# Performance work log

Measured on AMD Instinct MI355X. Metric: run time of the kernel, lower is better.

The kernel has to match this reference:

```python
import jax, jax.numpy as jnp
import numpy as np

EMBED_DIM = 384
HEADS = 6
HEAD_DIM = EMBED_DIM // HEADS
WINDOW = 64


def setup_inputs() -> dict:
    key = jax.random.key(0)
    ks = jax.random.split(key, 5)
    B, T = 128, 256
    s_attn = 1.0 / np.sqrt(EMBED_DIM)
    x = jax.random.normal(ks[0], (B, T, EMBED_DIM), dtype=jnp.float32)
    W_attn = jax.random.normal(ks[1], (EMBED_DIM, 3 * EMBED_DIM), dtype=jnp.float32) * s_attn
    b_attn = jax.random.normal(ks[2], (3 * EMBED_DIM,), dtype=jnp.float32) * 0.02
    W_proj = jax.random.normal(ks[3], (EMBED_DIM, EMBED_DIM), dtype=jnp.float32) * s_attn
    b_proj = jax.random.normal(ks[4], (EMBED_DIM,), dtype=jnp.float32) * 0.02
    return {"x": x, "W_attn": W_attn, "b_attn": b_attn, "W_proj": W_proj, "b_proj": b_proj}


def reference(x, W_attn, b_attn, W_proj, b_proj):
    B, T, C = x.shape
    qkv = x @ W_attn + b_attn  # [B,T,3C]
    q, k, v = jnp.split(qkv, 3, axis=-1)
    # [B, H, T, hd]
    q = q.reshape(B, T, HEADS, HEAD_DIM).transpose(0, 2, 1, 3)
    k = k.reshape(B, T, HEADS, HEAD_DIM).transpose(0, 2, 1, 3)
    v = v.reshape(B, T, HEADS, HEAD_DIM).transpose(0, 2, 1, 3)
    scale = 1.0 / np.sqrt(HEAD_DIM).astype(np.float32)
    att = jnp.einsum('bhqd,bhkd->bhqk', q, k) * scale
    i = jnp.arange(T)
    causal = i[:, None] >= i[None, :]
    local = jnp.abs(i[:, None] - i[None, :]) <= WINDOW
    mask = (causal & local)[None, None, :, :]
    att = jnp.where(mask, att, -jnp.inf)
    att = jax.nn.softmax(att, axis=-1)
    y = jnp.einsum('bhqk,bhkd->bhqd', att, v)
    y = y.transpose(0, 2, 1, 3).reshape(B, T, C)
    return y @ W_proj + b_proj
```

## Files before the change

### kernel.cpp

```cpp
#include <hip/hip_runtime.h>

#define B_SZ   128
#define T_SEQ  256
#define C_DIM  384
#define HEADS  6
#define HD     64
#define WIN    64

typedef __bf16 bf16x8 __attribute__((ext_vector_type(8)));
typedef float  f32x4  __attribute__((ext_vector_type(4)));

typedef __attribute__((address_space(3))) void lds_void;
typedef __attribute__((address_space(1))) void gbl_void;

__device__ __forceinline__ unsigned short f2bf(float f) {
  unsigned u = __float_as_uint(f);
  u += 0x7FFFu + ((u >> 16) & 1u);
  return (unsigned short)(u >> 16);
}


__global__ __launch_bounds__(256) void convert_pack_f32_bf16(
    const float* __restrict__ in, unsigned short* __restrict__ out) {
  const int tid = blockIdx.x * 256 + threadIdx.x;
  const int m   = tid / 48;
  const int rem = tid % 48;
  const int kc  = rem >> 2;
  const int u   = rem & 3;
  const float4 a = *(const float4*)(in + (size_t)m * 384 + kc * 32 + u * 8);
  const float4 b = *(const float4*)(in + (size_t)m * 384 + kc * 32 + u * 8 + 4);
  const int p = u ^ ((m & 7) >> 1);
  unsigned short* dst =
      out + ((size_t)(m >> 7) * 12 + kc) * 4096 + (m & 127) * 32 + p * 8;
  ushort4 o1, o2;
  o1.x = f2bf(a.x); o1.y = f2bf(a.y); o1.z = f2bf(a.z); o1.w = f2bf(a.w);
  o2.x = f2bf(b.x); o2.y = f2bf(b.y); o2.z = f2bf(b.z); o2.w = f2bf(b.w);
  *(ushort4*)dst = o1;
  *(ushort4*)(dst + 4) = o2;
}

__global__ __launch_bounds__(256) void transpose_convert_pack(
    const float* __restrict__ in, unsigned short* __restrict__ out,
    int K, int N) {
  __shared__ float tile[32][33];
  const int gx = blockIdx.x * 32;
  const int gy = blockIdx.y * 32;
  const int tx = threadIdx.x;
  const int ty = threadIdx.y;
#pragma unroll
  for (int r = ty; r < 32; r += 8)
    tile[r][tx] = in[(size_t)(gy + r) * N + gx + tx];
  __syncthreads();
  const int nkc = K >> 5;
#pragma unroll
  for (int r = ty; r < 32; r += 8) {
    const int n = gx + r;
    const int k = gy + tx;
    const int p = (((k >> 3) & 3) ^ ((n & 7) >> 1));
    out[((size_t)(n >> 7) * nkc + (k >> 5)) * 4096 + (n & 127) * 32 + p * 8 +
        (k & 7)] = f2bf(tile[tx][r]);
  }
}

template <bool OUT_BF16, int KK>
__global__ __launch_bounds__(256, 3) void gemm_mfma_bf16(
    const unsigned short* __restrict__ A,
    const unsigned short* __restrict__ Bt,
    const float* __restrict__ bias,
    void* __restrict__ Cv, int M, int N, int tiles_n) {
  __shared__ __attribute__((aligned(16))) char smem_raw[49152];
  float* ep = (float*)smem_raw;

  constexpr int NK = KK / 32;

  const int t    = threadIdx.x;
  const int lane = t & 63;
  const int w    = t >> 6;
  const int wr   = w >> 1;
  const int wc   = w & 1;

  const unsigned id    = blockIdx.x;
  const unsigned remap = (id & 7u) * (gridDim.x >> 3) + (id >> 3);
  const int by = remap / (unsigned)tiles_n;
  const int bx = remap % (unsigned)tiles_n;
  const int m0 = by * 128;
  const int n0 = bx * 128;

  const unsigned short* Atile = A  + (size_t)by * NK * 4096;
  const unsigned short* Btile = Bt + (size_t)bx * NK * 4096;

  const int m16  = lane & 15;
  const int quad = lane >> 4;
  const int cp   = (quad ^ ((m16 >> 1) & 3)) << 3;

  f32x4 acc[4][4];
#pragma unroll
  for (int i = 0; i < 4; ++i)
#pragma unroll
    for (int j = 0; j < 4; ++j) acc[i][j] = (f32x4){0.f, 0.f, 0.f, 0.f};

  auto stage = [&](int slot, int kc) {
    unsigned short* Ad = (unsigned short*)(smem_raw + slot * 16384);
    unsigned short* Bd = Ad + 128 * 32;
    const unsigned short* ta = Atile + (size_t)kc * 4096;
    const unsigned short* tb = Btile + (size_t)kc * 4096;
#pragma unroll
    for (int i = 0; i < 2; ++i) {
      const int inst = w * 2 + i;
      __builtin_amdgcn_global_load_lds(
          (const gbl_void*)(ta + inst * 512 + lane * 8),
          (lds_void*)(Ad + inst * 512), 16, 0, 0);
      __builtin_amdgcn_global_load_lds(
          (const gbl_void*)(tb + inst * 512 + lane * 8),
          (lds_void*)(Bd + inst * 512), 16, 0, 0);
    }
  };

  stage(0, 0);
  stage(1, 1);

#pragma unroll
  for (int kt = 0; kt < NK; ++kt) {
    if (kt + 1 < NK)
      asm volatile("s_waitcnt vmcnt(4) lgkmcnt(0)" ::: "memory");
    else
      asm volatile("s_waitcnt vmcnt(0) lgkmcnt(0)" ::: "memory");
    __builtin_amdgcn_s_barrier();
    __builtin_amdgcn_sched_barrier(0);

    if (kt + 2 < NK) stage((kt + 2) % 3, kt + 2);

    const unsigned short* Ac =
        (const unsigned short*)(smem_raw + (kt % 3) * 16384);
    const unsigned short* Bc = Ac + 128 * 32;

    bf16x8 af[4];
#pragma unroll
    for (int mt = 0; mt < 4; ++mt)
      af[mt] = *(const bf16x8*)(Ac + (size_t)(wr * 64 + mt * 16 + m16) * 32 + cp);
#pragma unroll
    for (int nt = 0; nt < 4; ++nt) {
      bf16x8 bfr = *(const bf16x8*)(Bc + (size_t)(wc * 64 + nt * 16 + m16) * 32 + cp);
#pragma unroll
      for (int mt = 0; mt < 4; ++mt)
        acc[mt][nt] = __builtin_amdgcn_mfma_f32_16x16x32_bf16(
            af[mt], bfr, acc[mt][nt], 0, 0, 0);
    }
  }
  __syncthreads();

  float bv[4];
#pragma unroll
  for (int nt = 0; nt < 4; ++nt) bv[nt] = bias[n0 + wc * 64 + nt * 16 + m16];

  const int which = bx / 3;
  const int hbase = (bx % 3) * 2;

#pragma unroll
  for (int p = 0; p < 2; ++p) {
    if (p) __syncthreads();
    if (wr == p) {
#pragma unroll
      for (int mt = 0; mt < 4; ++mt)
#pragma unroll
        for (int nt = 0; nt < 4; ++nt)
#pragma unroll
          for (int r = 0; r < 4; ++r)
            ep[(mt * 16 + quad * 4 + r) * 132 + wc * 64 + nt * 16 + m16] =
                acc[mt][nt][r] + bv[nt];
    }
    __syncthreads();
#pragma unroll
    for (int cc = 0; cc < 8; ++cc) {
      const int chunk = cc * 256 + t;
      const int row = chunk >> 5;
      const int c4  = chunk & 31;
      const int grow = m0 + p * 64 + row;
      if (OUT_BF16) {
        const int hh  = c4 >> 4;
        const int g16 = c4 & 15;
        const int s   = (which == 2) ? 0 : (row & 7);
        const int col = hh * 64 + ((((g16 >> 1) ^ s) << 3) | ((g16 & 1) << 2));
        f32x4 v = *(const f32x4*)(ep + row * 132 + col);
        ushort4 o;
        o.x = f2bf(v[0]); o.y = f2bf(v[1]); o.z = f2bf(v[2]); o.w = f2bf(v[3]);
        const int b_ = grow >> 8;
        const int tp = grow & 255;
        *(ushort4*)((unsigned short*)Cv +
                    ((size_t)((b_ * 3 + which) * HEADS + hbase + hh) * T_SEQ +
                     tp) * HD + g16 * 4) = o;
      } else {
        f32x4 v = *(const f32x4*)(ep + row * 132 + c4 * 4);
        const int gcol = n0 + c4 * 4;
        *(f32x4*)((float*)Cv + (size_t)grow * N + gcol) = v;
      }
    }
  }
}

#define PSTR 68
__global__ __launch_bounds__(256) void attn_mfma(
    const unsigned short* __restrict__ qkv, unsigned short* __restrict__ y) {
  __shared__ unsigned short Qs[64 * 64];
  __shared__ unsigned short Ks[64 * 64];
  __shared__ unsigned short Vt[64 * 64];
  __shared__ float Pw[4][16 * PSTR];

  const unsigned id  = blockIdx.x;
  const unsigned bid = (id & 7u) * (gridDim.x >> 3) + (id >> 3);
  const int qt  = bid & 3;
  const int h   = (bid >> 2) % HEADS;
  const int b   = bid / (4 * HEADS);
  const int t   = threadIdx.x;
  const int lane = t & 63;
  const int w    = t >> 6;
  const int quad = lane >> 4;
  const int m16  = lane & 15;
  const int sw   = m16 & 7;

  const unsigned short* Qpane =
      qkv + ((size_t)((b * 3 + 0) * HEADS + h) * T_SEQ) * HD;
  const unsigned short* Kpane =
      qkv + ((size_t)((b * 3 + 1) * HEADS + h) * T_SEQ) * HD;
  const unsigned short* Vpane =
      qkv + ((size_t)((b * 3 + 2) * HEADS + h) * T_SEQ) * HD;
  const int qg0 = qt * 64;

#pragma unroll
  for (int i = 0; i < 2; ++i) {
    const int inst = w * 2 + i;
    __builtin_amdgcn_global_load_lds(
        (const gbl_void*)(Qpane + (size_t)qg0 * HD + inst * 512 + lane * 8),
        (lds_void*)(Qs + inst * 512), 16, 0, 0);
  }

  float m_r[4], l_r[4];
  f32x4 yacc[4];
#pragma unroll
  for (int r = 0; r < 4; ++r) { m_r[r] = -1e30f; l_r[r] = 0.f; }
#pragma unroll
  for (int dt = 0; dt < 4; ++dt) yacc[dt] = (f32x4){0.f, 0.f, 0.f, 0.f};

  const int nchunks  = (qt == 0) ? 1 : 2;
  const int kb_first = (qt == 0) ? 0 : (qg0 - 64);
  const int qrow_base = qg0 + w * 16 + quad * 4;

  for (int ch = 0; ch < nchunks; ++ch) {
    const int kb = kb_first + ch * 64;

    __syncthreads();

#pragma unroll
    for (int i = 0; i < 2; ++i) {
      const int inst = w * 2 + i;
      __builtin_amdgcn_global_load_lds(
          (const gbl_void*)(Kpane + (size_t)kb * HD + inst * 512 + lane * 8),
          (lds_void*)(Ks + inst * 512), 16, 0, 0);
    }
    {
      const int vkey = t & 63;
      const int kc = vkey >> 3, ke = vkey & 7;
      const int vd0  = (t >> 6) * 16;
      const unsigned short* gv = Vpane + (size_t)(kb + vkey) * HD + vd0;
#pragma unroll
      for (int u = 0; u < 4; ++u) {
        ushort4 vv = *(const ushort4*)(gv + u * 4);
#pragma unroll
        for (int jj = 0; jj < 4; ++jj) {
          const int d = vd0 + u * 4 + jj;
          const unsigned short val =
              (jj == 0) ? vv.x : (jj == 1) ? vv.y : (jj == 2) ? vv.z : vv.w;
          Vt[d * 64 + ((kc ^ (d & 7)) << 3) + ke] = val;
        }
      }
    }
    __syncthreads();

    f32x4 sacc[4];
#pragma unroll
    for (int nt = 0; nt < 4; ++nt) sacc[nt] = (f32x4){0.f, 0.f, 0.f, 0.f};
#pragma unroll
    for (int ks = 0; ks < 64; ks += 32) {
      const int cp = (((ks >> 3) + quad) ^ sw) << 3;
      bf16x8 aq = *(const bf16x8*)(Qs + (size_t)(w * 16 + m16) * 64 + cp);
#pragma unroll
      for (int nt = 0; nt < 4; ++nt) {
        bf16x8 kf = *(const bf16x8*)(Ks + (size_t)(nt * 16 + m16) * 64 + cp);
        sacc[nt] = __builtin_amdgcn_mfma_f32_16x16x32_bf16(aq, kf, sacc[nt], 0, 0, 0);
      }
    }

    float mc[4] = {-1e30f, -1e30f, -1e30f, -1e30f};
#pragma unroll
    for (int nt = 0; nt < 4; ++nt) {
      const int kg = kb + nt * 16 + m16;
#pragma unroll
      for (int r = 0; r < 4; ++r) {
        const int qg = qrow_base + r;
        const bool valid = (kg <= qg) && (qg - kg <= WIN);
        const float sv = valid ? (sacc[nt][r] * 0.125f) : -1e30f;
        sacc[nt][r] = sv;
        mc[r] = fmaxf(mc[r], sv);
      }
    }
#pragma unroll
    for (int r = 0; r < 4; ++r) {
#pragma unroll
      for (int x = 1; x <= 8; x <<= 1) mc[r] = fmaxf(mc[r], __shfl_xor(mc[r], x));
    }

#pragma unroll
    for (int r = 0; r < 4; ++r) {
      const float mn    = fmaxf(m_r[r], mc[r]);
      const float alpha = __expf(m_r[r] - mn);
      m_r[r] = mn;
      l_r[r] *= alpha;
#pragma unroll
      for (int dt = 0; dt < 4; ++dt) yacc[dt][r] *= alpha;
      float ls = 0.f;
#pragma unroll
      for (int nt = 0; nt < 4; ++nt) {
        const float p = __expf(sacc[nt][r] - mn);
        sacc[nt][r] = p;
        ls += p;
      }
#pragma unroll
      for (int x = 1; x <= 8; x <<= 1) ls += __shfl_xor(ls, x);
      l_r[r] += ls;
    }

#pragma unroll
    for (int nt = 0; nt < 4; ++nt)
#pragma unroll
      for (int r = 0; r < 4; ++r)
        Pw[w][(quad * 4 + r) * PSTR + nt * 16 + m16] = sacc[nt][r];

#pragma unroll
    for (int ks = 0; ks < 64; ks += 32) {
      f32x4 pa = *(const f32x4*)(&Pw[w][m16 * PSTR + ks + quad * 8]);
      f32x4 pb = *(const f32x4*)(&Pw[w][m16 * PSTR + ks + quad * 8 + 4]);
      bf16x8 ap;
#pragma unroll
      for (int j = 0; j < 4; ++j) {
        ap[j]     = (__bf16)pa[j];
        ap[4 + j] = (__bf16)pb[j];
      }
      const int cp = (((ks >> 3) + quad) ^ sw) << 3;
#pragma unroll
      for (int dt = 0; dt < 4; ++dt) {
        bf16x8 vf = *(const bf16x8*)(Vt + (size_t)(dt * 16 + m16) * 64 + cp);
        yacc[dt] = __builtin_amdgcn_mfma_f32_16x16x32_bf16(ap, vf, yacc[dt], 0, 0, 0);
      }
    }
  }

  float* epy = &Pw[0][0];
  float inv[4];
#pragma unroll
  for (int r = 0; r < 4; ++r) inv[r] = 1.f / l_r[r];
#pragma unroll
  for (int dt = 0; dt < 4; ++dt)
#pragma unroll
    for (int r = 0; r < 4; ++r)
      epy[(w * 16 + quad * 4 + r) * PSTR + dt * 16 + m16] = yacc[dt][r] * inv[r];
  __syncthreads();
#pragma unroll
  for (int cc = 0; cc < 4; ++cc) {
    const int chunk = cc * 256 + t;
    const int row = chunk >> 4;
    const int c4  = chunk & 15;
    f32x4 v = *(const f32x4*)(epy + row * PSTR + c4 * 4);
    ushort4 o;
    o.x = f2bf(v[0]); o.y = f2bf(v[1]); o.z = f2bf(v[2]); o.w = f2bf(v[3]);
    const int m = b * T_SEQ + qg0 + row;
    const int c = h * HD + c4 * 4;
    const int kc = c >> 5;
    const int u  = (c >> 3) & 3;
    const int p  = u ^ ((m & 7) >> 1);
    *(ushort4*)(y + ((size_t)(m >> 7) * 12 + kc) * 4096 + (m & 127) * 32 +
                p * 8 + (c & 7)) = o;
  }
}

extern "C" void kernel_launch(void* const* d_in, const int* in_sizes, int n_in,
                              void* d_out, int out_size, void* d_ws, size_t ws_size,
                              hipStream_t stream) {
  const float* x      = (const float*)d_in[0];
  const float* W_attn = (const float*)d_in[1];
  const float* b_attn = (const float*)d_in[2];
  const float* W_proj = (const float*)d_in[3];
  const float* b_proj = (const float*)d_in[4];
  float* out = (float*)d_out;

  const int M = B_SZ * T_SEQ;

  unsigned short* qkv_b = (unsigned short*)d_ws;
  unsigned short* y_b   = qkv_b + (size_t)M * (3 * C_DIM);
  unsigned short* x_b   = y_b   + (size_t)M * C_DIM;
  unsigned short* Wa_t  = x_b   + (size_t)M * C_DIM;
  unsigned short* Wp_t  = Wa_t  + (size_t)(3 * C_DIM) * C_DIM;

  {
    convert_pack_f32_bf16<<<dim3(M * 48 / 256), 256, 0, stream>>>(x, x_b);
    transpose_convert_pack<<<dim3((3 * C_DIM) / 32, C_DIM / 32), dim3(32, 8), 0,
                             stream>>>(W_attn, Wa_t, C_DIM, 3 * C_DIM);
    transpose_convert_pack<<<dim3(C_DIM / 32, C_DIM / 32), dim3(32, 8), 0,
                             stream>>>(W_proj, Wp_t, C_DIM, C_DIM);
  }

  gemm_mfma_bf16<true, C_DIM><<<dim3(9 * (M / 128)), 256, 0, stream>>>(
      x_b, Wa_t, b_attn, qkv_b, M, 3 * C_DIM, 9);

  attn_mfma<<<dim3(B_SZ * HEADS * (T_SEQ / 64)), 256, 0, stream>>>(qkv_b, y_b);

  gemm_mfma_bf16<false, C_DIM><<<dim3(3 * (M / 128)), 256, 0, stream>>>(
      y_b, Wp_t, b_proj, out, M, C_DIM, 3);
}
```

Before: 201.8 us.

## Enlarge GEMM block tile to 256x128 with 512 threads sharing B tile

The GEMM kernels now use 512-thread blocks covering 256 rows by 128 columns, so each B tile loaded into LDS is reused by twice as many rows. The staging loop is redistributed over 8 waves, the LDS ring grows to 72 KB, and the epilogue now runs four row passes. This halves the grid size and the B-tile traffic per output, at the cost of more LDS per block and possibly lower occupancy. The 512,4 launch bound may not be reachable with this LDS usage, and fewer blocks may underfill the device for the smaller projection GEMM.

```diff
diff --git a/kernel.cpp b/kernel.cpp
--- a/kernel.cpp
+++ b/kernel.cpp
@@ -63,12 +63,12 @@
 }
 
 template <bool OUT_BF16, int KK>
-__global__ __launch_bounds__(256, 3) void gemm_mfma_bf16(
+__global__ __launch_bounds__(512, 4) void gemm_mfma_bf16(
     const unsigned short* __restrict__ A,
     const unsigned short* __restrict__ Bt,
     const float* __restrict__ bias,
     void* __restrict__ Cv, int M, int N, int tiles_n) {
-  __shared__ __attribute__((aligned(16))) char smem_raw[49152];
+  __shared__ __attribute__((aligned(16))) char smem_raw[73728];
   float* ep = (float*)smem_raw;
 
   constexpr int NK = KK / 32;
@@ -83,10 +83,11 @@
   const unsigned remap = (id & 7u) * (gridDim.x >> 3) + (id >> 3);
   const int by = remap / (unsigned)tiles_n;
   const int bx = remap % (unsigned)tiles_n;
-  const int m0 = by * 128;
+  const int m0 = by * 256;
   const int n0 = bx * 128;
 
-  const unsigned short* Atile = A  + (size_t)by * NK * 4096;
+  const unsigned short* Ap0 = A  + (size_t)(by * 2)     * NK * 4096;
+  const unsigned short* Ap1 = A  + (size_t)(by * 2 + 1) * NK * 4096;
   const unsigned short* Btile = Bt + (size_t)bx * NK * 4096;
 
   const int m16  = lane & 15;
@@ -100,19 +101,24 @@
     for (int j = 0; j < 4; ++j) acc[i][j] = (f32x4){0.f, 0.f, 0.f, 0.f};
 
   auto stage = [&](int slot, int kc) {
-    unsigned short* Ad = (unsigned short*)(smem_raw + slot * 16384);
-    unsigned short* Bd = Ad + 128 * 32;
-    const unsigned short* ta = Atile + (size_t)kc * 4096;
-    const unsigned short* tb = Btile + (size_t)kc * 4096;
-#pragma unroll
-    for (int i = 0; i < 2; ++i) {
-      const int inst = w * 2 + i;
-      __builtin_amdgcn_global_load_lds(
-          (const gbl_void*)(ta + inst * 512 + lane * 8),
-          (lds_void*)(Ad + inst * 512), 16, 0, 0);
-      __builtin_amdgcn_global_load_lds(
-          (const gbl_void*)(tb + inst * 512 + lane * 8),
-          (lds_void*)(Bd + inst * 512), 16, 0, 0);
+    unsigned short* As = (unsigned short*)(smem_raw + slot * 24576);
+    unsigned short* Bs = As + 256 * 32;
+#pragma unroll
+    for (int i = 0; i < 3; ++i) {
+      const int idx = w * 3 + i;
+      if (idx < 16) {
+        const unsigned short* src =
+            ((idx >> 3) ? Ap1 : Ap0) + (size_t)kc * 4096 + (idx & 7) * 512 +
+            lane * 8;
+        __builtin_amdgcn_global_load_lds((const gbl_void*)src,
+                                         (lds_void*)(As + idx * 512), 16, 0, 0);
+      } else {
+        const int sub = idx - 16;
+        const unsigned short* src =
+            Btile + (size_t)kc * 4096 + sub * 512 + lane * 8;
+        __builtin_amdgcn_global_load_lds((const gbl_void*)src,
+                                         (lds_void*)(Bs + sub * 512), 16, 0, 0);
+      }
     }
   };
 
@@ -122,7 +128,7 @@
 #pragma unroll
   for (int kt = 0; kt < NK; ++kt) {
     if (kt + 1 < NK)
-      asm volatile("s_waitcnt vmcnt(4) lgkmcnt(0)" ::: "memory");
+      asm volatile("s_waitcnt vmcnt(3) lgkmcnt(0)" ::: "memory");
     else
       asm volatile("s_waitcnt vmcnt(0) lgkmcnt(0)" ::: "memory");
     __builtin_amdgcn_s_barrier();
@@ -130,17 +136,17 @@
 
     if (kt + 2 < NK) stage((kt + 2) % 3, kt + 2);
 
-    const unsigned short* Ac =
-        (const unsigned short*)(smem_raw + (kt % 3) * 16384);
-    const unsigned short* Bc = Ac + 128 * 32;
+    const unsigned short* As =
+        (const unsigned short*)(smem_raw + (kt % 3) * 24576);
+    const unsigned short* Bs = As + 256 * 32;
 
     bf16x8 af[4];
 #pragma unroll
     for (int mt = 0; mt < 4; ++mt)
-      af[mt] = *(const bf16x8*)(Ac + (size_t)(wr * 64 + mt * 16 + m16) * 32 + cp);
+      af[mt] = *(const bf16x8*)(As + (size_t)(wr * 64 + mt * 16 + m16) * 32 + cp);
 #pragma unroll
     for (int nt = 0; nt < 4; ++nt) {
-      bf16x8 bfr = *(const bf16x8*)(Bc + (size_t)(wc * 64 + nt * 16 + m16) * 32 + cp);
+      bf16x8 bfr = *(const bf16x8*)(Bs + (size_t)(wc * 64 + nt * 16 + m16) * 32 + cp);
 #pragma unroll
       for (int mt = 0; mt < 4; ++mt)
         acc[mt][nt] = __builtin_amdgcn_mfma_f32_16x16x32_bf16(
@@ -157,7 +163,7 @@
   const int hbase = (bx % 3) * 2;
 
 #pragma unroll
-  for (int p = 0; p < 2; ++p) {
+  for (int p = 0; p < 4; ++p) {
     if (p) __syncthreads();
     if (wr == p) {
 #pragma unroll
@@ -171,8 +177,8 @@
     }
     __syncthreads();
 #pragma unroll
-    for (int cc = 0; cc < 8; ++cc) {
-      const int chunk = cc * 256 + t;
+    for (int cc = 0; cc < 4; ++cc) {
+      const int chunk = cc * 512 + t;
       const int row = chunk >> 5;
       const int c4  = chunk & 31;
       const int grow = m0 + p * 64 + row;
@@ -408,11 +414,11 @@
                              stream>>>(W_proj, Wp_t, C_DIM, C_DIM);
   }
 
-  gemm_mfma_bf16<true, C_DIM><<<dim3(9 * (M / 128)), 256, 0, stream>>>(
+  gemm_mfma_bf16<true, C_DIM><<<dim3(9 * (M / 256)), 512, 0, stream>>>(
       x_b, Wa_t, b_attn, qkv_b, M, 3 * C_DIM, 9);
 
   attn_mfma<<<dim3(B_SZ * HEADS * (T_SEQ / 64)), 256, 0, stream>>>(qkv_b, y_b);
 
-  gemm_mfma_bf16<false, C_DIM><<<dim3(3 * (M / 128)), 256, 0, stream>>>(
+  gemm_mfma_bf16<false, C_DIM><<<dim3(3 * (M / 256)), 512, 0, stream>>>(
       y_b, Wp_t, b_proj, out, M, C_DIM, 3);
 }
```

Result: faster. 189.3 us (-6.2%).
